# Kernel tuning notes

Measured on AMD Instinct MI355X. Metric: run time of the kernel, lower is better.

## Reference

```python
import jax, jax.numpy as jnp
import numpy as np

B, T = 4, 2048
OBS, ST = 512, 512
H, E = 8, 64

def setup_inputs() -> dict:
    key = jax.random.key(0)
    k1, k2, k3, k4, k5 = jax.random.split(key, 5)
    observe = jax.random.normal(k1, (B, T, OBS), dtype=jnp.float32)
    state = jax.random.normal(k2, (B, T, ST), dtype=jnp.float32)
    # nn.Linear weights (out, in) applied as x @ W.T; store transposed for einsum
    Wq = jax.random.normal(k3, (OBS, H * E), dtype=jnp.float32) * (1.0 / np.sqrt(OBS))
    Wk = jax.random.normal(k4, (ST, H * E), dtype=jnp.float32) * (1.0 / np.sqrt(ST))
    Wv = jax.random.normal(k5, (ST, H * E), dtype=jnp.float32) * (1.0 / np.sqrt(ST))
    merge_w = jnp.ones((1, H, E), dtype=jnp.float32)  # Merger weight, init fill_(1.0)
    return {"observe": observe, "state": state, "Wq": Wq, "Wk": Wk, "Wv": Wv, "merge_w": merge_w}

def reference(observe, state, Wq, Wk, Wv, merge_w):
    b, t, _ = observe.shape
    h, e = H, E
    scale = e ** 0.25
    q = (observe @ Wq).reshape(b, t, h, e).transpose(0, 2, 1, 3) / scale  # [b,h,t,e]
    k = (state @ Wk).reshape(b, t, h, e).transpose(0, 2, 1, 3) / scale
    v = (state @ Wv).reshape(b, t, h, e).transpose(0, 2, 1, 3)
    dot = jnp.einsum('bhqe,bhke->bhqk', q, k)  # [b,h,t,t]
    attn = jax.nn.softmax(dot, axis=-1)
    out = jnp.einsum('bhqk,bhke->bhqe', attn, v)  # [b,h,t,e]
    out = out.transpose(0, 2, 1, 3).reshape(b * t, h, e)  # [b*t,h,e]
    # Merger: softmax over head dim of learned weight, weighted head sum
    w = jax.nn.softmax(merge_w, axis=1)  # [1,h,e]
    return jnp.sum(w * out, axis=1)  # [b*t,e]
```

## Files before the change

kernel.cpp:

```cpp
#include <hip/hip_runtime.h>

#define B_ 4
#define T_ 2048
#define H_ 8
#define E_ 64
#define KDIM 512

typedef unsigned short ushort_t;
typedef __attribute__((ext_vector_type(4))) float f32x4;
typedef __attribute__((ext_vector_type(4))) int i32x4;
typedef __attribute__((ext_vector_type(8))) short s16x8;

#define QK_SCALE 0.42466043f

__device__ __forceinline__ ushort_t f2bf(float f) {
  unsigned u = __builtin_bit_cast(unsigned, f);
  u += 0x7fffu + ((u >> 16) & 1u);
  return (ushort_t)(u >> 16);
}
__device__ __forceinline__ unsigned pk2(float a, float b) {
  return (unsigned)f2bf(a) | ((unsigned)f2bf(b) << 16);
}
__device__ __forceinline__ void gl2lds16(const void* g, void* l) {
  __builtin_amdgcn_global_load_lds((const __attribute__((address_space(1))) unsigned*)g,
                                   (__attribute__((address_space(3))) unsigned*)l, 16, 0, 0);
}

__global__ void k_prep(const float* __restrict__ Wq, const float* __restrict__ Wk,
                       const float* __restrict__ Wv, ushort_t* __restrict__ wt) {
  int z = blockIdx.y;
  int tid = blockIdx.x * 256 + threadIdx.x;
  int k = tid >> 9, n = tid & 511;
  const float* W = (z == 0) ? Wq : (z == 1 ? Wk : Wv);
  float scale = (z < 2) ? QK_SCALE : 1.0f;
  wt[z * 262144 + n * 512 + k] = f2bf(W[k * 512 + n] * scale);
}

__global__ void k_wgt(const float* __restrict__ mw, float* __restrict__ wgt) {
  int e = threadIdx.x;
  float w[8], wmax = -1e30f;
  for (int h = 0; h < 8; h++) { w[h] = mw[h * 64 + e]; wmax = fmaxf(wmax, w[h]); }
  float wsum = 0.f;
  for (int h = 0; h < 8; h++) { w[h] = __expf(w[h] - wmax); wsum += w[h]; }
  float inv = 1.f / wsum;
  for (int h = 0; h < 8; h++) wgt[h * 64 + e] = w[h] * inv;
}

__global__ __launch_bounds__(256, 3) void k_proj(
    const float* __restrict__ obs, const float* __restrict__ st,
    const ushort_t* __restrict__ wt,
    ushort_t* __restrict__ qo, ushort_t* __restrict__ ko, ushort_t* __restrict__ vto) {
  __shared__ __align__(16) float    As[128 * 64];
  __shared__ __align__(16) ushort_t Bs[128 * 64];

  int id = blockIdx.x;
  int which = id >> 8;
  int nt = (id >> 6) & 3;
  int m0 = (id & 63) << 7, n0 = nt << 7;
  const float* X = (which == 0) ? obs : st;
  const ushort_t* W = wt + which * 262144;

  int tid = threadIdx.x, wave = tid >> 6, lane = tid & 63;
  int l15 = lane & 15, quad = lane >> 4;
  int wm = wave & 1, wn = wave >> 1;

  f32x4 acc[4][4];
  for (int i = 0; i < 4; i++)
    for (int j = 0; j < 4; j++) acc[i][j] = (f32x4){0.f, 0.f, 0.f, 0.f};

  int arl = lane >> 4, ap = lane & 15;
  int brl = lane >> 3, bp = lane & 7;

  for (int k0 = 0; k0 < KDIM; k0 += 64) {
    for (int ii = 0; ii < 8; ii++) {
      int r = wave * 32 + ii * 4 + arl;
      int lc = ap ^ ((r & 7) << 1);
      gl2lds16(X + (size_t)(m0 + r) * KDIM + k0 + lc * 4, &As[(wave * 32 + ii * 4) * 64]);
    }
    for (int ii = 0; ii < 4; ii++) {
      int r = wave * 32 + ii * 8 + brl;
      int lc = bp ^ (r & 7);
      gl2lds16(W + (size_t)(n0 + r) * KDIM + k0 + lc * 8, &Bs[(wave * 32 + ii * 8) * 64]);
    }
    __syncthreads();

    for (int kc = 0; kc < 2; kc++) {
      s16x8 a[4], b[4];
      for (int i = 0; i < 4; i++) {
        int mr = wm * 64 + i * 16 + l15;
        int pc = (kc * 8 + quad * 2) ^ ((l15 & 7) << 1);
        const float* ap2 = &As[mr * 64 + pc * 4];
        float4 x0 = *(const float4*)ap2;
        float4 x1 = *(const float4*)(ap2 + 4);
        i32x4 d;
        d[0] = (int)pk2(x0.x, x0.y);
        d[1] = (int)pk2(x0.z, x0.w);
        d[2] = (int)pk2(x1.x, x1.y);
        d[3] = (int)pk2(x1.z, x1.w);
        a[i] = __builtin_bit_cast(s16x8, d);
      }
      for (int j = 0; j < 4; j++) {
        int nr = wn * 64 + j * 16 + l15;
        int pc = (kc * 4 + quad) ^ (l15 & 7);
        b[j] = *(const s16x8*)&Bs[nr * 64 + pc * 8];
      }
      for (int i = 0; i < 4; i++)
        for (int j = 0; j < 4; j++)
          acc[i][j] = __builtin_amdgcn_mfma_f32_16x16x32_bf16(a[i], b[j], acc[i][j], 0, 0, 0);
    }
    __syncthreads();
  }

  for (int i = 0; i < 4; i++) {
    int grow = m0 + wm * 64 + i * 16 + quad * 4;
    for (int j = 0; j < 4; j++) {
      int gcol = n0 + wn * 64 + j * 16 + l15;
      int h = gcol >> 6, e = gcol & 63;
      for (int r = 0; r < 4; r++) {
        int row = grow + r;
        int bb = row >> 11, t = row & 2047;
        int bh = bb * H_ + h;
        ushort_t val = f2bf(acc[i][j][r]);
        if (which == 0)      qo[(((size_t)bh * T_ + t) << 6) + e] = val;
        else if (which == 1) ko[(((size_t)bh * T_ + t) << 6) + e] = val;
        else                 vto[(((size_t)bh << 6) + e) * T_ + t] = val;
      }
    }
  }
}

__global__ __launch_bounds__(256, 2) void k_attn(
    const ushort_t* __restrict__ q, const ushort_t* __restrict__ k,
    const ushort_t* __restrict__ vt, const float* __restrict__ wgt,
    float* __restrict__ out) {
  __shared__ __align__(16) ushort_t ks[128 * 64];
  __shared__ __align__(16) ushort_t vs[64 * 128];

  int id = blockIdx.x;
  int bh = id & 31, qt = id >> 5;
  int tid = threadIdx.x, wave = tid >> 6, lane = tid & 63;
  int l15 = lane & 15, quad = lane >> 4;

  s16x8 qf[2][2];
  for (int qs = 0; qs < 2; qs++) {
    const ushort_t* qp =
        q + (((size_t)bh * T_ + qt * 128 + wave * 32 + qs * 16 + l15) << 6) + quad * 8;
    qf[qs][0] = *(const s16x8*)qp;
    qf[qs][1] = *(const s16x8*)(qp + 32);
  }

  f32x4 o[2][4];
  for (int qs = 0; qs < 2; qs++)
    for (int j = 0; j < 4; j++) o[qs][j] = (f32x4){0.f, 0.f, 0.f, 0.f};
  float lsum[2] = {0.f, 0.f};

  int krl = lane >> 3, kp = lane & 7;
  int vrl = lane >> 4, vp = lane & 15;
  const ushort_t* kbase = k + ((size_t)bh * T_ << 6);
  const ushort_t* vbase = vt + ((size_t)bh << 6) * T_;

  for (int kt = 0; kt < 16; kt++) {
    for (int ii = 0; ii < 4; ii++) {
      int r = wave * 32 + ii * 8 + krl;
      int gkey = (r & 96) + (((r >> 2) & 3) << 3) + (((r >> 4) & 1) << 2) + (r & 3);
      int lc = kp ^ (r & 7);
      gl2lds16(kbase + ((size_t)(kt * 128 + gkey) << 6) + lc * 8,
               &ks[(wave * 32 + ii * 8) * 64]);
    }
    for (int ii = 0; ii < 4; ii++) {
      int e = wave * 16 + ii * 4 + vrl;
      int lc = vp ^ (e & 15);
      gl2lds16(vbase + (size_t)e * T_ + kt * 128 + lc * 8, &vs[(wave * 16 + ii * 4) * 128]);
    }
    __syncthreads();

    s16x8 bfr[2][4];
    for (int c = 0; c < 4; c++) {
      f32x4 s0[2], s1[2];
      for (int qs = 0; qs < 2; qs++) {
        s0[qs] = (f32x4){0.f, 0.f, 0.f, 0.f};
        s1[qs] = (f32x4){0.f, 0.f, 0.f, 0.f};
      }
      for (int kc = 0; kc < 2; kc++) {
        int pc = (kc * 4 + quad) ^ (l15 & 7);
        s16x8 k0f = *(const s16x8*)&ks[(c * 32 + l15) * 64 + pc * 8];
        s16x8 k1f = *(const s16x8*)&ks[(c * 32 + 16 + l15) * 64 + pc * 8];
        for (int qs = 0; qs < 2; qs++) {
          s0[qs] = __builtin_amdgcn_mfma_f32_16x16x32_bf16(k0f, qf[qs][kc], s0[qs], 0, 0, 0);
          s1[qs] = __builtin_amdgcn_mfma_f32_16x16x32_bf16(k1f, qf[qs][kc], s1[qs], 0, 0, 0);
        }
      }
      for (int qs = 0; qs < 2; qs++) {
        float p0 = exp2f(s0[qs][0]), p1 = exp2f(s0[qs][1]),
              p2 = exp2f(s0[qs][2]), p3 = exp2f(s0[qs][3]);
        float p4 = exp2f(s1[qs][0]), p5 = exp2f(s1[qs][1]),
              p6 = exp2f(s1[qs][2]), p7 = exp2f(s1[qs][3]);
        lsum[qs] += ((p0 + p1) + (p2 + p3)) + ((p4 + p5) + (p6 + p7));
        i32x4 d;
        d[0] = (int)pk2(p0, p1);
        d[1] = (int)pk2(p2, p3);
        d[2] = (int)pk2(p4, p5);
        d[3] = (int)pk2(p6, p7);
        bfr[qs][c] = __builtin_bit_cast(s16x8, d);
      }
    }

    for (int c = 0; c < 4; c++)
      for (int et = 0; et < 4; et++) {
        int pc = (c * 4 + quad) ^ l15;
        s16x8 vf = *(const s16x8*)&vs[(et * 16 + l15) * 128 + pc * 8];
        o[0][et] = __builtin_amdgcn_mfma_f32_16x16x32_bf16(vf, bfr[0][c], o[0][et], 0, 0, 0);
        o[1][et] = __builtin_amdgcn_mfma_f32_16x16x32_bf16(vf, bfr[1][c], o[1][et], 0, 0, 0);
      }
    __syncthreads();
  }

  int bb = bh >> 3, hh = bh & 7;
  for (int qs = 0; qs < 2; qs++) {
    float ls = lsum[qs];
    ls += __shfl_xor(ls, 16, 64);
    ls += __shfl_xor(ls, 32, 64);
    float inv = 1.f / ls;
    int t = qt * 128 + wave * 32 + qs * 16 + l15;
    for (int et = 0; et < 4; et++)
      for (int r = 0; r < 4; r++) {
        int e = et * 16 + quad * 4 + r;
        float val = o[qs][et][r] * inv * wgt[hh * 64 + e];
        atomicAdd(&out[(((size_t)bb * T_ + t) << 6) + e], val);
      }
  }
}

extern "C" void kernel_launch(void* const* d_in, const int* in_sizes, int n_in,
                              void* d_out, int out_size, void* d_ws, size_t ws_size,
                              hipStream_t stream) {
  const float* obs = (const float*)d_in[0];
  const float* st  = (const float*)d_in[1];
  const float* Wq  = (const float*)d_in[2];
  const float* Wk  = (const float*)d_in[3];
  const float* Wv  = (const float*)d_in[4];
  const float* mw  = (const float*)d_in[5];

  const size_t WS_NEEDED = 27262976;
  char* ws = (char*)d_ws;
  ushort_t* wt  = (ushort_t*)ws;
  float*    wgt = (float*)(ws + 1572864u);
  ushort_t* qo  = (ushort_t*)(ws + 2097152u);
  ushort_t* ko  = (ushort_t*)(ws + 10485760u);
  ushort_t* vto = (ushort_t*)(ws + 18874368u);
  float*    out = (float*)d_out;

  hipMemsetAsync(d_out, 0, (size_t)out_size * sizeof(float), stream);
  if (ws_size < WS_NEEDED) return;

  hipLaunchKernelGGL(k_prep, dim3(1024, 3), dim3(256), 0, stream, Wq, Wk, Wv, wt);
  hipLaunchKernelGGL(k_wgt,  dim3(1),       dim3(64),  0, stream, mw, wgt);
  hipLaunchKernelGGL(k_proj, dim3(768),     dim3(256), 0, stream, obs, st, wt, qo, ko, vto);
  hipLaunchKernelGGL(k_attn, dim3(512),     dim3(256), 0, stream, qo, ko, vto, wgt, out);
}
```

Measured before the change: 213.8 us.

## Double-buffer attention loads, MFMA row sums, wider projection tiles, tiled weight transpose

The attention kernel now double-buffers the K/V LDS tiles with precomputed pointers, so the next tile's global loads overlap compute and one barrier per iteration is removed. Softmax row sums move from VALU adds plus shuffles to an MFMA against a ones vector, and the exp results are converted to bf16 by truncation through a byte permute instead of round-to-nearest. The projection kernel uses 128x256 tiles with half the blocks, and computes V transposed so its transposed store is more contiguous. Weight prep becomes an LDS-tiled transpose for coalesced writes. The risks are lower occupancy in the projection, extra LDS in attention, and the truncating bf16 conversion adds a small bias to P and to the sums.

New measurement: 330.8 us. 1.55x slower.

```diff
diff --git a/kernel.cpp b/kernel.cpp
--- a/kernel.cpp
+++ b/kernel.cpp
@@ -21,6 +21,10 @@
 __device__ __forceinline__ unsigned pk2(float a, float b) {
   return (unsigned)f2bf(a) | ((unsigned)f2bf(b) << 16);
 }
+__device__ __forceinline__ unsigned pk2t(float a, float b) {
+  return __builtin_amdgcn_perm(__builtin_bit_cast(unsigned, b),
+                               __builtin_bit_cast(unsigned, a), 0x07060302u);
+}
 __device__ __forceinline__ void gl2lds16(const void* g, void* l) {
   __builtin_amdgcn_global_load_lds((const __attribute__((address_space(1))) unsigned*)g,
                                    (__attribute__((address_space(3))) unsigned*)l, 16, 0, 0);
@@ -28,12 +32,24 @@
 
 __global__ void k_prep(const float* __restrict__ Wq, const float* __restrict__ Wk,
                        const float* __restrict__ Wv, ushort_t* __restrict__ wt) {
-  int z = blockIdx.y;
-  int tid = blockIdx.x * 256 + threadIdx.x;
-  int k = tid >> 9, n = tid & 511;
+  __shared__ ushort_t tile[64][66];
+  int z = blockIdx.z;
   const float* W = (z == 0) ? Wq : (z == 1 ? Wk : Wv);
   float scale = (z < 2) ? QK_SCALE : 1.0f;
-  wt[z * 262144 + n * 512 + k] = f2bf(W[k * 512 + n] * scale);
+  int k0 = blockIdx.y << 6, n0 = blockIdx.x << 6;
+  int rr = threadIdx.x >> 6, cc = threadIdx.x & 63;
+  for (int p = 0; p < 16; p++) {
+    int kl = p * 4 + rr;
+    tile[cc][kl] = f2bf(W[(size_t)(k0 + kl) * 512 + n0 + cc] * scale);
+  }
+  __syncthreads();
+  int kp2 = threadIdx.x & 31, nr = threadIdx.x >> 5;
+  unsigned* wt32 = (unsigned*)(wt + (size_t)z * 262144);
+  for (int p = 0; p < 8; p++) {
+    int nl = p * 8 + nr;
+    unsigned val = (unsigned)tile[nl][kp2 * 2] | ((unsigned)tile[nl][kp2 * 2 + 1] << 16);
+    wt32[(size_t)(n0 + nl) * 256 + (k0 >> 1) + kp2] = val;
+  }
 }
 
 __global__ void k_wgt(const float* __restrict__ mw, float* __restrict__ wgt) {
@@ -46,17 +62,17 @@
   for (int h = 0; h < 8; h++) wgt[h * 64 + e] = w[h] * inv;
 }
 
-__global__ __launch_bounds__(256, 3) void k_proj(
+__global__ __launch_bounds__(256, 2) void k_proj(
     const float* __restrict__ obs, const float* __restrict__ st,
     const ushort_t* __restrict__ wt,
     ushort_t* __restrict__ qo, ushort_t* __restrict__ ko, ushort_t* __restrict__ vto) {
   __shared__ __align__(16) float    As[128 * 64];
-  __shared__ __align__(16) ushort_t Bs[128 * 64];
+  __shared__ __align__(16) ushort_t Bs[256 * 64];
 
   int id = blockIdx.x;
-  int which = id >> 8;
-  int nt = (id >> 6) & 3;
-  int m0 = (id & 63) << 7, n0 = nt << 7;
+  int which = id >> 7;
+  int nt = (id >> 6) & 1;
+  int m0 = (id & 63) << 7, n0 = nt << 8;
   const float* X = (which == 0) ? obs : st;
   const ushort_t* W = wt + which * 262144;
 
@@ -64,9 +80,9 @@
   int l15 = lane & 15, quad = lane >> 4;
   int wm = wave & 1, wn = wave >> 1;
 
-  f32x4 acc[4][4];
+  f32x4 acc[4][8];
   for (int i = 0; i < 4; i++)
-    for (int j = 0; j < 4; j++) acc[i][j] = (f32x4){0.f, 0.f, 0.f, 0.f};
+    for (int j = 0; j < 8; j++) acc[i][j] = (f32x4){0.f, 0.f, 0.f, 0.f};
 
   int arl = lane >> 4, ap = lane & 15;
   int brl = lane >> 3, bp = lane & 7;
@@ -77,15 +93,15 @@
       int lc = ap ^ ((r & 7) << 1);
       gl2lds16(X + (size_t)(m0 + r) * KDIM + k0 + lc * 4, &As[(wave * 32 + ii * 4) * 64]);
     }
-    for (int ii = 0; ii < 4; ii++) {
-      int r = wave * 32 + ii * 8 + brl;
+    for (int ii = 0; ii < 8; ii++) {
+      int r = wave * 64 + ii * 8 + brl;
       int lc = bp ^ (r & 7);
-      gl2lds16(W + (size_t)(n0 + r) * KDIM + k0 + lc * 8, &Bs[(wave * 32 + ii * 8) * 64]);
+      gl2lds16(W + (size_t)(n0 + r) * KDIM + k0 + lc * 8, &Bs[(wave * 64 + ii * 8) * 64]);
     }
     __syncthreads();
 
     for (int kc = 0; kc < 2; kc++) {
-      s16x8 a[4], b[4];
+      s16x8 a[4], b[8];
       for (int i = 0; i < 4; i++) {
         int mr = wm * 64 + i * 16 + l15;
         int pc = (kc * 8 + quad * 2) ^ ((l15 & 7) << 1);
@@ -99,31 +115,50 @@
         d[3] = (int)pk2(x1.z, x1.w);
         a[i] = __builtin_bit_cast(s16x8, d);
       }
-      for (int j = 0; j < 4; j++) {
-        int nr = wn * 64 + j * 16 + l15;
+      for (int j = 0; j < 8; j++) {
+        int nr = wn * 128 + j * 16 + l15;
         int pc = (kc * 4 + quad) ^ (l15 & 7);
         b[j] = *(const s16x8*)&Bs[nr * 64 + pc * 8];
       }
-      for (int i = 0; i < 4; i++)
-        for (int j = 0; j < 4; j++)
-          acc[i][j] = __builtin_amdgcn_mfma_f32_16x16x32_bf16(a[i], b[j], acc[i][j], 0, 0, 0);
+      if (which == 2) {
+        for (int i = 0; i < 4; i++)
+          for (int j = 0; j < 8; j++)
+            acc[i][j] = __builtin_amdgcn_mfma_f32_16x16x32_bf16(b[j], a[i], acc[i][j], 0, 0, 0);
+      } else {
+        for (int i = 0; i < 4; i++)
+          for (int j = 0; j < 8; j++)
+            acc[i][j] = __builtin_amdgcn_mfma_f32_16x16x32_bf16(a[i], b[j], acc[i][j], 0, 0, 0);
+      }
     }
     __syncthreads();
   }
 
-  for (int i = 0; i < 4; i++) {
-    int grow = m0 + wm * 64 + i * 16 + quad * 4;
-    for (int j = 0; j < 4; j++) {
-      int gcol = n0 + wn * 64 + j * 16 + l15;
-      int h = gcol >> 6, e = gcol & 63;
-      for (int r = 0; r < 4; r++) {
-        int row = grow + r;
-        int bb = row >> 11, t = row & 2047;
-        int bh = bb * H_ + h;
-        ushort_t val = f2bf(acc[i][j][r]);
-        if (which == 0)      qo[(((size_t)bh * T_ + t) << 6) + e] = val;
-        else if (which == 1) ko[(((size_t)bh * T_ + t) << 6) + e] = val;
-        else                 vto[(((size_t)bh << 6) + e) * T_ + t] = val;
+  if (which != 2) {
+    ushort_t* dst = (which == 0) ? qo : ko;
+    for (int i = 0; i < 4; i++) {
+      int grow = m0 + wm * 64 + i * 16 + quad * 4;
+      for (int j = 0; j < 8; j++) {
+        int gcol = n0 + wn * 128 + j * 16 + l15;
+        int h = gcol >> 6, e = gcol & 63;
+        for (int r = 0; r < 4; r++) {
+          int row = grow + r;
+          int bb = row >> 11, t = row & 2047;
+          int bh = bb * H_ + h;
+          dst[(((size_t)bh * T_ + t) << 6) + e] = f2bf(acc[i][j][r]);
+        }
+      }
+    }
+  } else {
+    for (int i = 0; i < 4; i++) {
+      int row = m0 + wm * 64 + i * 16 + l15;
+      int bb = row >> 11, t = row & 2047;
+      for (int j = 0; j < 8; j++) {
+        for (int r = 0; r < 4; r++) {
+          int gcol = n0 + wn * 128 + j * 16 + quad * 4 + r;
+          int h = gcol >> 6, e = gcol & 63;
+          int bh = bb * H_ + h;
+          vto[((size_t)(bh << 6) + e) * T_ + t] = f2bf(acc[i][j][r]);
+        }
       }
     }
   }
@@ -133,8 +168,8 @@
     const ushort_t* __restrict__ q, const ushort_t* __restrict__ k,
     const ushort_t* __restrict__ vt, const float* __restrict__ wgt,
     float* __restrict__ out) {
-  __shared__ __align__(16) ushort_t ks[128 * 64];
-  __shared__ __align__(16) ushort_t vs[64 * 128];
+  __shared__ __align__(16) ushort_t ks[2][128 * 64];
+  __shared__ __align__(16) ushort_t vs[2][64 * 128];
 
   int id = blockIdx.x;
   int bh = id & 31, qt = id >> 5;
@@ -152,27 +187,42 @@
   f32x4 o[2][4];
   for (int qs = 0; qs < 2; qs++)
     for (int j = 0; j < 4; j++) o[qs][j] = (f32x4){0.f, 0.f, 0.f, 0.f};
-  float lsum[2] = {0.f, 0.f};
+  f32x4 lacc[2] = {(f32x4){0.f, 0.f, 0.f, 0.f}, (f32x4){0.f, 0.f, 0.f, 0.f}};
+  const s16x8 ones = {16256, 16256, 16256, 16256, 16256, 16256, 16256, 16256};
 
   int krl = lane >> 3, kp = lane & 7;
   int vrl = lane >> 4, vp = lane & 15;
   const ushort_t* kbase = k + ((size_t)bh * T_ << 6);
   const ushort_t* vbase = vt + ((size_t)bh << 6) * T_;
-
+  const ushort_t* kptr[4];
+  const ushort_t* vptr[4];
+  for (int ii = 0; ii < 4; ii++) {
+    int r = wave * 32 + ii * 8 + krl;
+    int gkey = (r & 96) + (((r >> 2) & 3) << 3) + (((r >> 4) & 1) << 2) + (r & 3);
+    int lc = kp ^ (r & 7);
+    kptr[ii] = kbase + ((size_t)gkey << 6) + lc * 8;
+    int e = wave * 16 + ii * 4 + vrl;
+    int lcv = vp ^ (e & 15);
+    vptr[ii] = vbase + (size_t)e * T_ + lcv * 8;
+  }
+
+#define STAGE(buf)                                                        \
+  do {                                                                    \
+    for (int ii = 0; ii < 4; ii++) {                                      \
+      gl2lds16(kptr[ii], &ks[buf][(wave * 32 + ii * 8) * 64]);            \
+      gl2lds16(vptr[ii], &vs[buf][(wave * 16 + ii * 4) * 128]);           \
+      kptr[ii] += 128 * 64;                                               \
+      vptr[ii] += 128;                                                    \
+    }                                                                     \
+  } while (0)
+
+  STAGE(0);
   for (int kt = 0; kt < 16; kt++) {
-    for (int ii = 0; ii < 4; ii++) {
-      int r = wave * 32 + ii * 8 + krl;
-      int gkey = (r & 96) + (((r >> 2) & 3) << 3) + (((r >> 4) & 1) << 2) + (r & 3);
-      int lc = kp ^ (r & 7);
-      gl2lds16(kbase + ((size_t)(kt * 128 + gkey) << 6) + lc * 8,
-               &ks[(wave * 32 + ii * 8) * 64]);
-    }
-    for (int ii = 0; ii < 4; ii++) {
-      int e = wave * 16 + ii * 4 + vrl;
-      int lc = vp ^ (e & 15);
-      gl2lds16(vbase + (size_t)e * T_ + kt * 128 + lc * 8, &vs[(wave * 16 + ii * 4) * 128]);
-    }
+    __builtin_amdgcn_s_waitcnt(0x0F70);
     __syncthreads();
+    if (kt < 15) STAGE((kt + 1) & 1);
+    const ushort_t* ksb = ks[kt & 1];
+    const ushort_t* vsb = vs[kt & 1];
 
     s16x8 bfr[2][4];
     for (int c = 0; c < 4; c++) {
@@ -183,44 +233,39 @@
       }
       for (int kc = 0; kc < 2; kc++) {
         int pc = (kc * 4 + quad) ^ (l15 & 7);
-        s16x8 k0f = *(const s16x8*)&ks[(c * 32 + l15) * 64 + pc * 8];
-        s16x8 k1f = *(const s16x8*)&ks[(c * 32 + 16 + l15) * 64 + pc * 8];
+        s16x8 k0f = *(const s16x8*)&ksb[(c * 32 + l15) * 64 + pc * 8];
+        s16x8 k1f = *(const s16x8*)&ksb[(c * 32 + 16 + l15) * 64 + pc * 8];
         for (int qs = 0; qs < 2; qs++) {
           s0[qs] = __builtin_amdgcn_mfma_f32_16x16x32_bf16(k0f, qf[qs][kc], s0[qs], 0, 0, 0);
           s1[qs] = __builtin_amdgcn_mfma_f32_16x16x32_bf16(k1f, qf[qs][kc], s1[qs], 0, 0, 0);
         }
       }
       for (int qs = 0; qs < 2; qs++) {
-        float p0 = exp2f(s0[qs][0]), p1 = exp2f(s0[qs][1]),
-              p2 = exp2f(s0[qs][2]), p3 = exp2f(s0[qs][3]);
-        float p4 = exp2f(s1[qs][0]), p5 = exp2f(s1[qs][1]),
-              p6 = exp2f(s1[qs][2]), p7 = exp2f(s1[qs][3]);
-        lsum[qs] += ((p0 + p1) + (p2 + p3)) + ((p4 + p5) + (p6 + p7));
         i32x4 d;
-        d[0] = (int)pk2(p0, p1);
-        d[1] = (int)pk2(p2, p3);
-        d[2] = (int)pk2(p4, p5);
-        d[3] = (int)pk2(p6, p7);
+        d[0] = (int)pk2t(exp2f(s0[qs][0]), exp2f(s0[qs][1]));
+        d[1] = (int)pk2t(exp2f(s0[qs][2]), exp2f(s0[qs][3]));
+        d[2] = (int)pk2t(exp2f(s1[qs][0]), exp2f(s1[qs][1]));
+        d[3] = (int)pk2t(exp2f(s1[qs][2]), exp2f(s1[qs][3]));
         bfr[qs][c] = __builtin_bit_cast(s16x8, d);
       }
     }
 
-    for (int c = 0; c < 4; c++)
+    for (int c = 0; c < 4; c++) {
+      lacc[0] = __builtin_amdgcn_mfma_f32_16x16x32_bf16(ones, bfr[0][c], lacc[0], 0, 0, 0);
+      lacc[1] = __builtin_amdgcn_mfma_f32_16x16x32_bf16(ones, bfr[1][c], lacc[1], 0, 0, 0);
       for (int et = 0; et < 4; et++) {
         int pc = (c * 4 + quad) ^ l15;
-        s16x8 vf = *(const s16x8*)&vs[(et * 16 + l15) * 128 + pc * 8];
+        s16x8 vf = *(const s16x8*)&vsb[(et * 16 + l15) * 128 + pc * 8];
         o[0][et] = __builtin_amdgcn_mfma_f32_16x16x32_bf16(vf, bfr[0][c], o[0][et], 0, 0, 0);
         o[1][et] = __builtin_amdgcn_mfma_f32_16x16x32_bf16(vf, bfr[1][c], o[1][et], 0, 0, 0);
       }
-    __syncthreads();
-  }
+    }
+  }
+#undef STAGE
 
   int bb = bh >> 3, hh = bh & 7;
   for (int qs = 0; qs < 2; qs++) {
-    float ls = lsum[qs];
-    ls += __shfl_xor(ls, 16, 64);
-    ls += __shfl_xor(ls, 32, 64);
-    float inv = 1.f / ls;
+    float inv = 1.f / lacc[qs][0];
     int t = qt * 128 + wave * 32 + qs * 16 + l15;
     for (int et = 0; et < 4; et++)
       for (int r = 0; r < 4; r++) {
@@ -253,8 +298,8 @@
   hipMemsetAsync(d_out, 0, (size_t)out_size * sizeof(float), stream);
   if (ws_size < WS_NEEDED) return;
 
-  hipLaunchKernelGGL(k_prep, dim3(1024, 3), dim3(256), 0, stream, Wq, Wk, Wv, wt);
+  hipLaunchKernelGGL(k_prep, dim3(8, 8, 3), dim3(256), 0, stream, Wq, Wk, Wv, wt);
   hipLaunchKernelGGL(k_wgt,  dim3(1),       dim3(64),  0, stream, mw, wgt);
-  hipLaunchKernelGGL(k_proj, dim3(768),     dim3(256), 0, stream, obs, st, wt, qo, ko, vto);
+  hipLaunchKernelGGL(k_proj, dim3(384),     dim3(256), 0, stream, obs, st, wt, qo, ko, vto);
   hipLaunchKernelGGL(k_attn, dim3(512),     dim3(256), 0, stream, qo, ko, vto, wgt, out);
 }
```
